# Optimization experiments

Measured on AMD Instinct MI355X. Metric: run time of the kernel, lower is better.

The kernel has to match this reference:

```python
import jax, jax.numpy as jnp
import numpy as np

B, S, D, H = 2, 2048, 1024, 16
HD = D // H  # head_dim = 64


def setup_inputs() -> dict:
    key = jax.random.key(0)
    ks = jax.random.split(key, 12)
    scale = 1.0 / np.sqrt(D)
    inp = {
        "query": jax.random.normal(ks[0], (B, S, D), jnp.float32),
        "key": jax.random.normal(ks[1], (B, S, D), jnp.float32),
        "value": jax.random.normal(ks[2], (B, S, D), jnp.float32),
        # causal mask, True = masked out; shape [B, q_len, k_len]
        "mask": jnp.broadcast_to(
            jnp.triu(jnp.ones((S, S), jnp.bool_), k=1), (B, S, S)
        ),
        "Wq": jax.random.normal(ks[3], (D, D), jnp.float32) * scale,
        "bq": jnp.zeros((D,), jnp.float32),
        "Wk": jax.random.normal(ks[4], (D, D), jnp.float32) * scale,
        "bk": jnp.zeros((D,), jnp.float32),
        "Wv": jax.random.normal(ks[5], (D, D), jnp.float32) * scale,
        "bv": jnp.zeros((D,), jnp.float32),
        "Wo": jax.random.normal(ks[6], (D, D), jnp.float32) * scale,
        "bo": jnp.zeros((D,), jnp.float32),
    }
    return inp


def _split_heads(x):
    b, s, _ = x.shape
    return x.reshape(b, s, H, HD).transpose(0, 2, 1, 3)  # [B,H,S,HD]


def reference(query, key, value, mask, Wq, bq, Wk, bk, Wv, bv, Wo, bo):
    # Linear layers use torch convention: y = x @ W.T + b, W is [out, in]
    q = _split_heads(query @ Wq.T + bq)
    k = _split_heads(key @ Wk.T + bk)
    v = _split_heads(value @ Wv.T + bv)
    scores = jnp.einsum("bhqd,bhkd->bhqk", q, k) / jnp.sqrt(jnp.float32(HD))
    # normalized mask [B,1,q,k]; True means masked
    scores = jnp.where(mask[:, None, :, :], jnp.finfo(scores.dtype).min, scores)
    attn = jax.nn.softmax(scores, axis=-1)  # dropout is identity in eval
    ctx = jnp.einsum("bhqk,bhkd->bhqd", attn, v)
    merged = ctx.transpose(0, 2, 1, 3).reshape(query.shape[0], -1, D)
    out = merged @ Wo.T + bo
    return out
```

## Files before the change

kernel.cpp:

```cpp
#include <hip/hip_runtime.h>

#define B_ 2
#define S_ 2048
#define D_ 1024
#define H_ 16
#define HD_ 64
#define M_ (B_ * S_)

typedef __bf16 bf16x8 __attribute__((ext_vector_type(8)));
typedef float f32x4 __attribute__((ext_vector_type(4)));

__device__ inline unsigned short f2bf(float f) {
    unsigned int u = __builtin_bit_cast(unsigned int, f);
    u += 0x7fffu + ((u >> 16) & 1u);
    return (unsigned short)(u >> 16);
}

__device__ inline unsigned int cvt_pk_bf16(float lo, float hi) {
    unsigned int r;
    asm("v_cvt_pk_bf16_f32 %0, %1, %2" : "=v"(r) : "v"(lo), "v"(hi));
    return r;
}

__device__ inline float fexp2(float x) { return __builtin_amdgcn_exp2f(x); }

__device__ inline void barrier_fence() {
    asm volatile("" ::: "memory");
    __builtin_amdgcn_s_barrier();
    asm volatile("" ::: "memory");
}

__device__ inline void async_ld16(const unsigned short* g, unsigned short* l) {
    __builtin_amdgcn_global_load_lds(
        (const __attribute__((address_space(1))) unsigned int*)g,
        (__attribute__((address_space(3))) unsigned int*)l, 16, 0, 0);
}

__global__ __launch_bounds__(256) void cvt_all(
    const float* __restrict__ i0, const float* __restrict__ i1, const float* __restrict__ i2,
    const float* __restrict__ i3, const float* __restrict__ i4, const float* __restrict__ i5,
    const float* __restrict__ i6,
    unsigned short* __restrict__ o0, unsigned short* __restrict__ o1, unsigned short* __restrict__ o2,
    unsigned short* __restrict__ o3, unsigned short* __restrict__ o4, unsigned short* __restrict__ o5,
    unsigned short* __restrict__ o6, int nbig, int nsmall) {
    int z = blockIdx.y;
    const float* in = (z == 0) ? i0 : (z == 1) ? i1 : (z == 2) ? i2 : (z == 3) ? i3
                     : (z == 4) ? i4 : (z == 5) ? i5 : i6;
    unsigned short* out = (z == 0) ? o0 : (z == 1) ? o1 : (z == 2) ? o2 : (z == 3) ? o3
                         : (z == 4) ? o4 : (z == 5) ? o5 : o6;
    int n = (z < 3) ? nbig : nsmall;
    int i = (blockIdx.x * 256 + threadIdx.x) * 4;
    if (i >= n) return;
    float4 v = *(const float4*)(in + i);
    ushort4 o;
    o.x = f2bf(v.x); o.y = f2bf(v.y); o.z = f2bf(v.z); o.w = f2bf(v.w);
    *(ushort4*)(out + i) = o;
}

__device__ inline void gemm_compute(const unsigned short* __restrict__ A,
                                    const unsigned short* __restrict__ W,
                                    int K, int m0, int n0,
                                    unsigned short* As0, unsigned short* As1,
                                    unsigned short* Bs0, unsigned short* Bs1,
                                    f32x4 acc[4][4]) {
    const int t = threadIdx.x;
    const int lane = t & 63, wave = t >> 6;
    const int ml = lane & 15, quad = lane >> 4;
    const int wr = (wave >> 1) * 64, wc = (wave & 1) * 64;
    const int srow = lane >> 2;
    const int schunk = (lane & 3) ^ ((lane >> 4) & 3);

    const f32x4 zero = {0.f, 0.f, 0.f, 0.f};
    for (int i = 0; i < 4; i++)
        for (int j = 0; j < 4; j++) acc[i][j] = zero;

    const int niter = K >> 5;

    auto issue = [&](int kt, unsigned short* As, unsigned short* Bs) {
        int k0 = kt << 5;
        for (int i = 0; i < 2; i++) {
            int r = wave * 32 + i * 16;
            async_ld16(A + (size_t)(m0 + r + srow) * K + k0 + schunk * 8, As + r * 32);
            async_ld16(W + (size_t)(n0 + r + srow) * K + k0 + schunk * 8, Bs + r * 32);
        }
    };

    issue(0, As0, Bs0);
    issue(1, As1, Bs1);
    asm volatile("s_waitcnt vmcnt(4)" ::: "memory");
    barrier_fence();

    for (int kt = 0; kt < niter; kt++) {
        unsigned short* As = (kt & 1) ? As1 : As0;
        unsigned short* Bs = (kt & 1) ? Bs1 : Bs0;

        bf16x8 af[4], bfr[4];
        for (int i = 0; i < 4; i++)
            af[i] = *(const bf16x8*)(As + (wr + i * 16 + ml) * 32 + ((quad ^ (ml >> 2)) << 3));
        for (int j = 0; j < 4; j++)
            bfr[j] = *(const bf16x8*)(Bs + (wc + j * 16 + ml) * 32 + ((quad ^ (ml >> 2)) << 3));
        for (int i = 0; i < 4; i++)
            for (int j = 0; j < 4; j++)
                acc[i][j] = __builtin_amdgcn_mfma_f32_16x16x32_bf16(af[i], bfr[j], acc[i][j], 0, 0, 0);

        barrier_fence();
        if (kt + 2 < niter) {
            issue(kt + 2, As, Bs);
            asm volatile("s_waitcnt vmcnt(4)" ::: "memory");
        } else {
            asm volatile("s_waitcnt vmcnt(0)" ::: "memory");
        }
        barrier_fence();
    }
}

__global__ __launch_bounds__(256) void gemm_qkv(
    const unsigned short* __restrict__ xq, const unsigned short* __restrict__ xk,
    const unsigned short* __restrict__ xv,
    const unsigned short* __restrict__ wq, const unsigned short* __restrict__ wk,
    const unsigned short* __restrict__ wv,
    const float* __restrict__ bq, const float* __restrict__ bk, const float* __restrict__ bv,
    unsigned short* __restrict__ oq, unsigned short* __restrict__ ok,
    unsigned short* __restrict__ ov) {
    extern __shared__ __align__(16) unsigned short smem[];
    unsigned short* As0 = smem;
    unsigned short* As1 = smem + 4096;
    unsigned short* Bs0 = smem + 8192;
    unsigned short* Bs1 = smem + 12288;

    int f = blockIdx.x + (blockIdx.y << 3) + (blockIdx.z << 8);
    int l = (f & 7) * 96 + (f >> 3);
    int bx = l & 7, by = (l >> 3) & 31, z = l >> 8;

    const unsigned short *A, *W;
    const float* bias;
    unsigned short* out;
    if (z == 0) { A = xq; W = wq; bias = bq; out = oq; }
    else if (z == 1) { A = xk; W = wk; bias = bk; out = ok; }
    else { A = xv; W = wv; bias = bv; out = ov; }

    int m0 = by * 128, n0 = bx * 128;
    f32x4 acc[4][4];
    gemm_compute(A, W, D_, m0, n0, As0, As1, Bs0, Bs1, acc);

    const int t = threadIdx.x, lane = t & 63, wave = t >> 6;
    const int ml = lane & 15, quad = lane >> 4;
    const int wr = (wave >> 1) * 64, wc = (wave & 1) * 64;

    unsigned short* Cs = smem;
    const float sc = (z == 0) ? 0.1803368801111204f : 1.0f;
    for (int i = 0; i < 4; i++)
        for (int j = 0; j < 4; j++) {
            int col = wc + j * 16 + ml;
            float bb = bias[n0 + col];
            for (int rg = 0; rg < 4; rg++) {
                int row = wr + i * 16 + quad * 4 + rg;
                unsigned short v = f2bf((acc[i][j][rg] + bb) * sc);
                if (z < 2) Cs[row * 136 + col] = v;
                else       Cs[col * 136 + row] = v;
            }
        }
    __syncthreads();

    const int r = t >> 1, hf = t & 1;
    if (z < 2) {
        unsigned short* dst = out + (size_t)(m0 + r) * D_ + n0 + hf * 64;
        const unsigned short* src = Cs + r * 136 + hf * 64;
        for (int i = 0; i < 8; i++)
            *(uint4*)(dst + i * 8) = *(const uint4*)(src + i * 8);
    } else {
        int n = n0 + r, h = n >> 6, d = n & 63;
        int b = m0 >> 11, s0 = m0 & 2047;
        unsigned short* dst = ov + ((size_t)((b * H_ + h) * 64 + d)) * S_ + s0 + hf * 64;
        const unsigned short* src = Cs + r * 136 + hf * 64;
        for (int i = 0; i < 8; i++)
            *(uint4*)(dst + i * 8) = *(const uint4*)(src + i * 8);
    }
}

__global__ __launch_bounds__(256) void gemm_out(const unsigned short* __restrict__ A,
                                                const unsigned short* __restrict__ W,
                                                const float* __restrict__ bias,
                                                float* __restrict__ out) {
    __shared__ unsigned short As0[128 * 32], As1[128 * 32], Bs0[128 * 32], Bs1[128 * 32];

    int f = blockIdx.x + (blockIdx.y << 3);
    int l = (f & 7) * 32 + (f >> 3);
    int bx = l & 7, by = l >> 3;

    int m0 = by * 128, n0 = bx * 128;
    f32x4 acc[4][4];
    gemm_compute(A, W, D_, m0, n0, As0, As1, Bs0, Bs1, acc);

    const int t = threadIdx.x, lane = t & 63, wave = t >> 6;
    const int ml = lane & 15, quad = lane >> 4;
    const int wr = (wave >> 1) * 64, wc = (wave & 1) * 64;
    for (int i = 0; i < 4; i++)
        for (int j = 0; j < 4; j++) {
            int n = n0 + wc + j * 16 + ml;
            float bb = bias[n];
            for (int rg = 0; rg < 4; rg++) {
                int m = m0 + wr + i * 16 + quad * 4 + rg;
                out[(size_t)m * D_ + n] = acc[i][j][rg] + bb;
            }
        }
}

__global__ __launch_bounds__(256, 2) void attn_kernel(const unsigned short* __restrict__ qm,
                                                      const unsigned short* __restrict__ km,
                                                      const unsigned short* __restrict__ vt,
                                                      unsigned short* __restrict__ ctx) {
    __shared__ unsigned short Ks[2][128 * 64];
    __shared__ unsigned short Vs[2][64 * 128];

    const int g = blockIdx.x >> 5;
    const int ip = (g < 8) ? (15 - g) : (g - 8);
    const int bh = blockIdx.x & 31;
    const int b = bh >> 4, h = bh & 15;
    const size_t vbase = (size_t)bh * S_ * 64;
    const int t = threadIdx.x, lane = t & 63, wave = t >> 6;
    const int ml = lane & 15, quad = lane >> 4;
    const int lrow = lane >> 3;
    const int gchunk = (lane & 7) ^ lrow;
    const int vrow = lane >> 4;
    const int q0 = ip * 128;
    const int nt = ip + 1;

    bf16x8 qfA[2], qfB[2];
    {
        int qrow = q0 + wave * 16 + ml;
        const unsigned short* qp = qm + (size_t)(b * S_ + qrow) * D_ + h * 64;
        qfA[0] = *(const bf16x8*)(qp + quad * 8);
        qfA[1] = *(const bf16x8*)(qp + 32 + quad * 8);
        const unsigned short* qp2 = qp + (size_t)64 * D_;
        qfB[0] = *(const bf16x8*)(qp2 + quad * 8);
        qfB[1] = *(const bf16x8*)(qp2 + 32 + quad * 8);
    }

    auto issue_K = [&](int kt, int bb) {
        for (int i = 0; i < 4; i++) {
            int r = wave * 32 + i * 8;
            async_ld16(km + (size_t)(b * S_ + kt * 128 + r + lrow) * D_ + h * 64 + gchunk * 8,
                       Ks[bb] + r * 64);
        }
    };
    auto issue_V = [&](int kt, int bb) {
        for (int i = 0; i < 4; i++) {
            int dd = wave * 16 + i * 4;
            int d = dd + vrow;
            async_ld16(vt + vbase + (size_t)d * S_ + kt * 128 + (((lane & 15) ^ (d & 15)) << 3),
                       Vs[bb] + dd * 128);
        }
    };

    const f32x4 zero = {0.f, 0.f, 0.f, 0.f};
    f32x4 accA[4], accB[4];
    for (int j = 0; j < 4; j++) { accA[j] = zero; accB[j] = zero; }
    float mA = -INFINITY, mB = -INFINITY, lpA = 0.f, lpB = 0.f;

    issue_K(0, 0);
    issue_V(0, 0);
    asm volatile("s_waitcnt vmcnt(0)" ::: "memory");
    barrier_fence();

    for (int kt = 0; kt < nt; kt++) {
        const int buf = kt & 1;
        if (kt + 1 < nt) { issue_K(kt + 1, buf ^ 1); issue_V(kt + 1, buf ^ 1); }

        f32x4 sA[8], sB[8];
        for (int n = 0; n < 8; n++) { sA[n] = zero; sB[n] = zero; }
        __builtin_amdgcn_s_setprio(1);
        for (int n = 0; n < 8; n++)
            for (int kk = 0; kk < 2; kk++) {
                bf16x8 kf = *(const bf16x8*)(Ks[buf] + (n * 16 + ml) * 64 +
                                             (((kk * 4 + quad) ^ (ml & 7)) << 3));
                sA[n] = __builtin_amdgcn_mfma_f32_16x16x32_bf16(kf, qfA[kk], sA[n], 0, 0, 0);
                sB[n] = __builtin_amdgcn_mfma_f32_16x16x32_bf16(kf, qfB[kk], sB[n], 0, 0, 0);
            }
        __builtin_amdgcn_s_setprio(0);

        const int qidxA = q0 + wave * 16 + ml;
        const int qidxB = qidxA + 64;
        if (kt == nt - 1) {
            for (int n = 0; n < 8; n++)
                for (int rg = 0; rg < 4; rg++) {
                    int kidx = kt * 128 + n * 16 + quad * 4 + rg;
                    if (kidx > qidxA) sA[n][rg] = -3.0e38f;
                    if (kidx > qidxB) sB[n][rg] = -3.0e38f;
                }
        }

        float a0 = fmaxf(fmaxf(sA[0][0], sA[0][1]), fmaxf(sA[0][2], sA[0][3]));
        float a1 = fmaxf(fmaxf(sA[1][0], sA[1][1]), fmaxf(sA[1][2], sA[1][3]));
        float a2 = fmaxf(fmaxf(sA[2][0], sA[2][1]), fmaxf(sA[2][2], sA[2][3]));
        float a3 = fmaxf(fmaxf(sA[3][0], sA[3][1]), fmaxf(sA[3][2], sA[3][3]));
        float a4 = fmaxf(fmaxf(sA[4][0], sA[4][1]), fmaxf(sA[4][2], sA[4][3]));
        float a5 = fmaxf(fmaxf(sA[5][0], sA[5][1]), fmaxf(sA[5][2], sA[5][3]));
        float a6 = fmaxf(fmaxf(sA[6][0], sA[6][1]), fmaxf(sA[6][2], sA[6][3]));
        float a7 = fmaxf(fmaxf(sA[7][0], sA[7][1]), fmaxf(sA[7][2], sA[7][3]));
        float mxA = fmaxf(fmaxf(fmaxf(a0, a1), fmaxf(a2, a3)),
                          fmaxf(fmaxf(a4, a5), fmaxf(a6, a7)));
        float b0 = fmaxf(fmaxf(sB[0][0], sB[0][1]), fmaxf(sB[0][2], sB[0][3]));
        float b1 = fmaxf(fmaxf(sB[1][0], sB[1][1]), fmaxf(sB[1][2], sB[1][3]));
        float b2 = fmaxf(fmaxf(sB[2][0], sB[2][1]), fmaxf(sB[2][2], sB[2][3]));
        float b3 = fmaxf(fmaxf(sB[3][0], sB[3][1]), fmaxf(sB[3][2], sB[3][3]));
        float b4 = fmaxf(fmaxf(sB[4][0], sB[4][1]), fmaxf(sB[4][2], sB[4][3]));
        float b5 = fmaxf(fmaxf(sB[5][0], sB[5][1]), fmaxf(sB[5][2], sB[5][3]));
        float b6 = fmaxf(fmaxf(sB[6][0], sB[6][1]), fmaxf(sB[6][2], sB[6][3]));
        float b7 = fmaxf(fmaxf(sB[7][0], sB[7][1]), fmaxf(sB[7][2], sB[7][3]));
        float mxB = fmaxf(fmaxf(fmaxf(b0, b1), fmaxf(b2, b3)),
                          fmaxf(fmaxf(b4, b5), fmaxf(b6, b7)));

        if (!__all((mxA <= mA + 4.0f) & (mxB <= mB + 4.0f))) {
            float mcA = fmaxf(mxA, __shfl_xor(mxA, 16));
            mcA = fmaxf(mcA, __shfl_xor(mcA, 32));
            mcA = fmaxf(mA, mcA);
            float alA = fexp2(mA - mcA);
            mA = mcA;
            float mcB = fmaxf(mxB, __shfl_xor(mxB, 16));
            mcB = fmaxf(mcB, __shfl_xor(mcB, 32));
            mcB = fmaxf(mB, mcB);
            float alB = fexp2(mB - mcB);
            mB = mcB;
            float aTA[4], aTB[4];
            for (int rg = 0; rg < 4; rg++) {
                aTA[rg] = __shfl(alA, quad * 4 + rg);
                aTB[rg] = __shfl(alB, quad * 4 + rg);
            }
            for (int j = 0; j < 4; j++)
                for (int rg = 0; rg < 4; rg++) {
                    accA[j][rg] *= aTA[rg];
                    accB[j][rg] *= aTB[rg];
                }
            lpA *= alA;
            lpB *= alB;
        }

        for (int n = 0; n < 8; n++)
            for (int rg = 0; rg < 4; rg++) {
                sA[n][rg] = fexp2(sA[n][rg] - mA);
                sB[n][rg] = fexp2(sB[n][rg] - mB);
            }
        {
            float r0 = 0.f, r1 = 0.f;
            for (int n = 0; n < 8; n++) {
                r0 += (sA[n][0] + sA[n][1]) + (sA[n][2] + sA[n][3]);
                r1 += (sB[n][0] + sB[n][1]) + (sB[n][2] + sB[n][3]);
            }
            lpA += r0;
            lpB += r1;
        }

        __builtin_amdgcn_s_setprio(1);
        for (int n2 = 0; n2 < 4; n2++) {
            union { bf16x8 v; unsigned int w[4]; } pkA, pkB;
            pkA.w[0] = cvt_pk_bf16(sA[2 * n2][0], sA[2 * n2][1]);
            pkA.w[1] = cvt_pk_bf16(sA[2 * n2][2], sA[2 * n2][3]);
            pkA.w[2] = cvt_pk_bf16(sA[2 * n2 + 1][0], sA[2 * n2 + 1][1]);
            pkA.w[3] = cvt_pk_bf16(sA[2 * n2 + 1][2], sA[2 * n2 + 1][3]);
            pkB.w[0] = cvt_pk_bf16(sB[2 * n2][0], sB[2 * n2][1]);
            pkB.w[1] = cvt_pk_bf16(sB[2 * n2][2], sB[2 * n2][3]);
            pkB.w[2] = cvt_pk_bf16(sB[2 * n2 + 1][0], sB[2 * n2 + 1][1]);
            pkB.w[3] = cvt_pk_bf16(sB[2 * n2 + 1][2], sB[2 * n2 + 1][3]);
            const int c0 = 4 * n2 + (quad >> 1);
            const int qo = (quad & 1) << 2;
            for (int j = 0; j < 4; j++) {
                int row = j * 16 + ml;
                union { bf16x8 v; uint2 d2[2]; } vv;
                vv.d2[0] = *(const uint2*)(Vs[buf] + row * 128 + (((c0 ^ (row & 15)) << 3) + qo));
                vv.d2[1] = *(const uint2*)(Vs[buf] + row * 128 + ((((c0 + 2) ^ (row & 15)) << 3) + qo));
                accA[j] = __builtin_amdgcn_mfma_f32_16x16x32_bf16(pkA.v, vv.v, accA[j], 0, 0, 0);
                accB[j] = __builtin_amdgcn_mfma_f32_16x16x32_bf16(pkB.v, vv.v, accB[j], 0, 0, 0);
            }
        }
        __builtin_amdgcn_s_setprio(0);

        asm volatile("s_waitcnt vmcnt(0)" ::: "memory");
        barrier_fence();
    }

    float lcA = lpA + __shfl_xor(lpA, 16);
    lcA += __shfl_xor(lcA, 32);
    float lcB = lpB + __shfl_xor(lpB, 16);
    lcB += __shfl_xor(lcB, 32);
    float invA[4], invB[4];
    for (int rg = 0; rg < 4; rg++) {
        invA[rg] = __builtin_amdgcn_rcpf(__shfl(lcA, quad * 4 + rg));
        invB[rg] = __builtin_amdgcn_rcpf(__shfl(lcB, quad * 4 + rg));
    }
    for (int j = 0; j < 4; j++) {
        int d = j * 16 + ml;
        for (int rg = 0; rg < 4; rg++) {
            int srow = q0 + wave * 16 + quad * 4 + rg;
            ctx[((size_t)(b * S_ + srow)) * D_ + h * 64 + d] = f2bf(accA[j][rg] * invA[rg]);
            ctx[((size_t)(b * S_ + srow + 64)) * D_ + h * 64 + d] = f2bf(accB[j][rg] * invB[rg]);
        }
    }
}

extern "C" void kernel_launch(void* const* d_in, const int* in_sizes, int n_in,
                              void* d_out, int out_size, void* d_ws, size_t ws_size,
                              hipStream_t stream) {
    const float* query = (const float*)d_in[0];
    const float* key_ = (const float*)d_in[1];
    const float* value = (const float*)d_in[2];
    const float* Wq = (const float*)d_in[4];
    const float* bq = (const float*)d_in[5];
    const float* Wk = (const float*)d_in[6];
    const float* bk = (const float*)d_in[7];
    const float* Wv = (const float*)d_in[8];
    const float* bv = (const float*)d_in[9];
    const float* Wo = (const float*)d_in[10];
    const float* bo = (const float*)d_in[11];
    float* out = (float*)d_out;

    const size_t XE = (size_t)M_ * D_;
    const size_t WE = (size_t)D_ * D_;
    char* ws = (char*)d_ws;
    unsigned short* xq = (unsigned short*)ws; ws += XE * 2;
    unsigned short* xk = (unsigned short*)ws; ws += XE * 2;
    unsigned short* xv = (unsigned short*)ws; ws += XE * 2;
    unsigned short* wqb = (unsigned short*)ws; ws += WE * 2;
    unsigned short* wkb = (unsigned short*)ws; ws += WE * 2;
    unsigned short* wvb = (unsigned short*)ws; ws += WE * 2;
    unsigned short* wob = (unsigned short*)ws; ws += WE * 2;
    unsigned short* qmb = (unsigned short*)ws; ws += XE * 2;
    unsigned short* kmb = (unsigned short*)ws; ws += XE * 2;
    unsigned short* vt = (unsigned short*)ws; ws += XE * 2;
    unsigned short* ctx = (unsigned short*)ws; ws += XE * 2;

    cvt_all<<<dim3(XE / 1024, 7), 256, 0, stream>>>(
        query, key_, value, Wq, Wk, Wv, Wo,
        xq, xk, xv, wqb, wkb, wvb, wob, (int)XE, (int)WE);

    gemm_qkv<<<dim3(D_ / 128, M_ / 128, 3), 256, 34816, stream>>>(
        xq, xk, xv, wqb, wkb, wvb, bq, bk, bv, qmb, kmb, vt);

    attn_kernel<<<dim3(512), 256, 0, stream>>>(qmb, kmb, vt, ctx);

    gemm_out<<<dim3(D_ / 128, M_ / 128), 256, 0, stream>>>(ctx, wob, bo, out);
}
```

Baseline: 245.6 us.

## Fuse fp32-to-bf16 conversion into GEMM loads, dropping the separate cvt kernel

Removes the standalone conversion kernel that wrote bf16 copies of the inputs and weights. The QKV and output GEMMs now load fp32 directly into registers, pack to bf16 with v_cvt_pk_bf16, and write to LDS through a register-staged double buffer. The output GEMM keeps async global-to-LDS loads for the bf16 context. This saves a kernel launch and a write-then-reread round trip, but the GEMMs now read twice as many bytes and give up direct-to-LDS async loads, so latency hiding inside the main loop may get worse.

```diff
diff --git a/kernel.cpp b/kernel.cpp
--- a/kernel.cpp
+++ b/kernel.cpp
@@ -30,39 +30,38 @@
     asm volatile("" ::: "memory");
 }
 
+__device__ inline void order_fence() {
+    asm volatile("" ::: "memory");
+}
+
 __device__ inline void async_ld16(const unsigned short* g, unsigned short* l) {
     __builtin_amdgcn_global_load_lds(
         (const __attribute__((address_space(1))) unsigned int*)g,
         (__attribute__((address_space(3))) unsigned int*)l, 16, 0, 0);
 }
 
-__global__ __launch_bounds__(256) void cvt_all(
-    const float* __restrict__ i0, const float* __restrict__ i1, const float* __restrict__ i2,
-    const float* __restrict__ i3, const float* __restrict__ i4, const float* __restrict__ i5,
-    const float* __restrict__ i6,
-    unsigned short* __restrict__ o0, unsigned short* __restrict__ o1, unsigned short* __restrict__ o2,
-    unsigned short* __restrict__ o3, unsigned short* __restrict__ o4, unsigned short* __restrict__ o5,
-    unsigned short* __restrict__ o6, int nbig, int nsmall) {
-    int z = blockIdx.y;
-    const float* in = (z == 0) ? i0 : (z == 1) ? i1 : (z == 2) ? i2 : (z == 3) ? i3
-                     : (z == 4) ? i4 : (z == 5) ? i5 : i6;
-    unsigned short* out = (z == 0) ? o0 : (z == 1) ? o1 : (z == 2) ? o2 : (z == 3) ? o3
-                         : (z == 4) ? o4 : (z == 5) ? o5 : o6;
-    int n = (z < 3) ? nbig : nsmall;
-    int i = (blockIdx.x * 256 + threadIdx.x) * 4;
-    if (i >= n) return;
-    float4 v = *(const float4*)(in + i);
-    ushort4 o;
-    o.x = f2bf(v.x); o.y = f2bf(v.y); o.z = f2bf(v.z); o.w = f2bf(v.w);
-    *(ushort4*)(out + i) = o;
-}
-
-__device__ inline void gemm_compute(const unsigned short* __restrict__ A,
-                                    const unsigned short* __restrict__ W,
-                                    int K, int m0, int n0,
-                                    unsigned short* As0, unsigned short* As1,
-                                    unsigned short* Bs0, unsigned short* Bs1,
-                                    f32x4 acc[4][4]) {
+struct f32x8r { float4 lo, hi; };
+__device__ inline f32x8r ldg8(const float* p) {
+    f32x8r r;
+    r.lo = *(const float4*)p;
+    r.hi = *(const float4*)(p + 4);
+    return r;
+}
+__device__ inline uint4 pk8(const f32x8r& v) {
+    uint4 o;
+    o.x = cvt_pk_bf16(v.lo.x, v.lo.y);
+    o.y = cvt_pk_bf16(v.lo.z, v.lo.w);
+    o.z = cvt_pk_bf16(v.hi.x, v.hi.y);
+    o.w = cvt_pk_bf16(v.hi.z, v.hi.w);
+    return o;
+}
+
+__device__ inline void gemm_compute_f32(const float* __restrict__ A,
+                                        const float* __restrict__ W,
+                                        int K, int m0, int n0,
+                                        unsigned short* As0, unsigned short* As1,
+                                        unsigned short* Bs0, unsigned short* Bs1,
+                                        f32x4 acc[4][4]) {
     const int t = threadIdx.x;
     const int lane = t & 63, wave = t >> 6;
     const int ml = lane & 15, quad = lane >> 4;
@@ -76,23 +75,43 @@
 
     const int niter = K >> 5;
 
-    auto issue = [&](int kt, unsigned short* As, unsigned short* Bs) {
+    const float* pA0 = A + (size_t)(m0 + wave * 32 + srow) * K + schunk * 8;
+    const float* pA1 = pA0 + (size_t)16 * K;
+    const float* pW0 = W + (size_t)(n0 + wave * 32 + srow) * K + schunk * 8;
+    const float* pW1 = pW0 + (size_t)16 * K;
+    const int woff = wave * 32 * 32 + lane * 8;
+
+    f32x8r rA0, rA1, rW0, rW1;
+    auto LOAD = [&](int kt) {
         int k0 = kt << 5;
-        for (int i = 0; i < 2; i++) {
-            int r = wave * 32 + i * 16;
-            async_ld16(A + (size_t)(m0 + r + srow) * K + k0 + schunk * 8, As + r * 32);
-            async_ld16(W + (size_t)(n0 + r + srow) * K + k0 + schunk * 8, Bs + r * 32);
-        }
-    };
-
-    issue(0, As0, Bs0);
-    issue(1, As1, Bs1);
-    asm volatile("s_waitcnt vmcnt(4)" ::: "memory");
+        rA0 = ldg8(pA0 + k0);
+        rA1 = ldg8(pA1 + k0);
+        rW0 = ldg8(pW0 + k0);
+        rW1 = ldg8(pW1 + k0);
+    };
+    auto WRITE = [&](unsigned short* As, unsigned short* Bs) {
+        *(uint4*)(As + woff) = pk8(rA0);
+        *(uint4*)(As + woff + 512) = pk8(rA1);
+        *(uint4*)(Bs + woff) = pk8(rW0);
+        *(uint4*)(Bs + woff + 512) = pk8(rW1);
+    };
+
+    LOAD(0);
+    asm volatile("s_waitcnt vmcnt(0)" ::: "memory");
+    WRITE(As0, Bs0);
+    LOAD(1);
+    asm volatile("s_waitcnt lgkmcnt(0)" ::: "memory");
     barrier_fence();
 
     for (int kt = 0; kt < niter; kt++) {
         unsigned short* As = (kt & 1) ? As1 : As0;
         unsigned short* Bs = (kt & 1) ? Bs1 : Bs0;
+
+        if (kt + 1 < niter) {
+            asm volatile("s_waitcnt vmcnt(0)" ::: "memory");
+            WRITE((kt & 1) ? As0 : As1, (kt & 1) ? Bs0 : Bs1);
+            if (kt + 2 < niter) LOAD(kt + 2);
+        }
 
         bf16x8 af[4], bfr[4];
         for (int i = 0; i < 4; i++)
@@ -103,22 +122,96 @@
             for (int j = 0; j < 4; j++)
                 acc[i][j] = __builtin_amdgcn_mfma_f32_16x16x32_bf16(af[i], bfr[j], acc[i][j], 0, 0, 0);
 
+        asm volatile("s_waitcnt lgkmcnt(0)" ::: "memory");
         barrier_fence();
-        if (kt + 2 < niter) {
-            issue(kt + 2, As, Bs);
-            asm volatile("s_waitcnt vmcnt(4)" ::: "memory");
-        } else {
+    }
+}
+
+__device__ inline void gemm_compute_mix(const unsigned short* __restrict__ A,
+                                        const float* __restrict__ W,
+                                        int K, int m0, int n0,
+                                        unsigned short* As0, unsigned short* As1,
+                                        unsigned short* Bs0, unsigned short* Bs1,
+                                        f32x4 acc[4][4]) {
+    const int t = threadIdx.x;
+    const int lane = t & 63, wave = t >> 6;
+    const int ml = lane & 15, quad = lane >> 4;
+    const int wr = (wave >> 1) * 64, wc = (wave & 1) * 64;
+    const int srow = lane >> 2;
+    const int schunk = (lane & 3) ^ ((lane >> 4) & 3);
+
+    const f32x4 zero = {0.f, 0.f, 0.f, 0.f};
+    for (int i = 0; i < 4; i++)
+        for (int j = 0; j < 4; j++) acc[i][j] = zero;
+
+    const int niter = K >> 5;
+
+    const float* pW0 = W + (size_t)(n0 + wave * 32 + srow) * K + schunk * 8;
+    const float* pW1 = pW0 + (size_t)16 * K;
+    const int woff = wave * 32 * 32 + lane * 8;
+
+    f32x8r rW0, rW1;
+    auto LOADW = [&](int kt) {
+        int k0 = kt << 5;
+        rW0 = ldg8(pW0 + k0);
+        rW1 = ldg8(pW1 + k0);
+    };
+    auto WRITEW = [&](unsigned short* Bs) {
+        *(uint4*)(Bs + woff) = pk8(rW0);
+        *(uint4*)(Bs + woff + 512) = pk8(rW1);
+    };
+    auto issueA = [&](int kt, unsigned short* As) {
+        int k0 = kt << 5;
+        for (int i = 0; i < 2; i++) {
+            int r = wave * 32 + i * 16;
+            async_ld16(A + (size_t)(m0 + r + srow) * K + k0 + schunk * 8, As + r * 32);
+        }
+    };
+
+    LOADW(0);
+    asm volatile("s_waitcnt vmcnt(0)" ::: "memory");
+    WRITEW(Bs0);
+    issueA(0, As0);
+    order_fence();
+    LOADW(1);
+    asm volatile("s_waitcnt vmcnt(4)" ::: "memory");
+    asm volatile("s_waitcnt lgkmcnt(0)" ::: "memory");
+    barrier_fence();
+
+    for (int kt = 0; kt < niter; kt++) {
+        unsigned short* As = (kt & 1) ? As1 : As0;
+        unsigned short* Bs = (kt & 1) ? Bs1 : Bs0;
+
+        const bool more = (kt + 1 < niter);
+        if (more) {
             asm volatile("s_waitcnt vmcnt(0)" ::: "memory");
-        }
+            WRITEW((kt & 1) ? Bs0 : Bs1);
+            issueA(kt + 1, (kt & 1) ? As0 : As1);
+            order_fence();
+            if (kt + 2 < niter) LOADW(kt + 2);
+        }
+
+        bf16x8 af[4], bfr[4];
+        for (int i = 0; i < 4; i++)
+            af[i] = *(const bf16x8*)(As + (wr + i * 16 + ml) * 32 + ((quad ^ (ml >> 2)) << 3));
+        for (int j = 0; j < 4; j++)
+            bfr[j] = *(const bf16x8*)(Bs + (wc + j * 16 + ml) * 32 + ((quad ^ (ml >> 2)) << 3));
+        for (int i = 0; i < 4; i++)
+            for (int j = 0; j < 4; j++)
+                acc[i][j] = __builtin_amdgcn_mfma_f32_16x16x32_bf16(af[i], bfr[j], acc[i][j], 0, 0, 0);
+
+        if (more && kt + 2 < niter) asm volatile("s_waitcnt vmcnt(4)" ::: "memory");
+        else                        asm volatile("s_waitcnt vmcnt(0)" ::: "memory");
+        asm volatile("s_waitcnt lgkmcnt(0)" ::: "memory");
         barrier_fence();
     }
 }
 
 __global__ __launch_bounds__(256) void gemm_qkv(
-    const unsigned short* __restrict__ xq, const unsigned short* __restrict__ xk,
-    const unsigned short* __restrict__ xv,
-    const unsigned short* __restrict__ wq, const unsigned short* __restrict__ wk,
-    const unsigned short* __restrict__ wv,
+    const float* __restrict__ xq, const float* __restrict__ xk,
+    const float* __restrict__ xv,
+    const float* __restrict__ wq, const float* __restrict__ wk,
+    const float* __restrict__ wv,
     const float* __restrict__ bq, const float* __restrict__ bk, const float* __restrict__ bv,
     unsigned short* __restrict__ oq, unsigned short* __restrict__ ok,
     unsigned short* __restrict__ ov) {
@@ -132,7 +225,7 @@
     int l = (f & 7) * 96 + (f >> 3);
     int bx = l & 7, by = (l >> 3) & 31, z = l >> 8;
 
-    const unsigned short *A, *W;
+    const float *A, *W;
     const float* bias;
     unsigned short* out;
     if (z == 0) { A = xq; W = wq; bias = bq; out = oq; }
@@ -141,7 +234,7 @@
 
     int m0 = by * 128, n0 = bx * 128;
     f32x4 acc[4][4];
-    gemm_compute(A, W, D_, m0, n0, As0, As1, Bs0, Bs1, acc);
+    gemm_compute_f32(A, W, D_, m0, n0, As0, As1, Bs0, Bs1, acc);
 
     const int t = threadIdx.x, lane = t & 63, wave = t >> 6;
     const int ml = lane & 15, quad = lane >> 4;
@@ -179,7 +272,7 @@
 }
 
 __global__ __launch_bounds__(256) void gemm_out(const unsigned short* __restrict__ A,
-                                                const unsigned short* __restrict__ W,
+                                                const float* __restrict__ W,
                                                 const float* __restrict__ bias,
                                                 float* __restrict__ out) {
     __shared__ unsigned short As0[128 * 32], As1[128 * 32], Bs0[128 * 32], Bs1[128 * 32];
@@ -190,7 +283,7 @@
 
     int m0 = by * 128, n0 = bx * 128;
     f32x4 acc[4][4];
-    gemm_compute(A, W, D_, m0, n0, As0, As1, Bs0, Bs1, acc);
+    gemm_compute_mix(A, W, D_, m0, n0, As0, As1, Bs0, Bs1, acc);
 
     const int t = threadIdx.x, lane = t & 63, wave = t >> 6;
     const int ml = lane & 15, quad = lane >> 4;
@@ -415,28 +508,16 @@
     float* out = (float*)d_out;
 
     const size_t XE = (size_t)M_ * D_;
-    const size_t WE = (size_t)D_ * D_;
     char* ws = (char*)d_ws;
-    unsigned short* xq = (unsigned short*)ws; ws += XE * 2;
-    unsigned short* xk = (unsigned short*)ws; ws += XE * 2;
-    unsigned short* xv = (unsigned short*)ws; ws += XE * 2;
-    unsigned short* wqb = (unsigned short*)ws; ws += WE * 2;
-    unsigned short* wkb = (unsigned short*)ws; ws += WE * 2;
-    unsigned short* wvb = (unsigned short*)ws; ws += WE * 2;
-    unsigned short* wob = (unsigned short*)ws; ws += WE * 2;
     unsigned short* qmb = (unsigned short*)ws; ws += XE * 2;
     unsigned short* kmb = (unsigned short*)ws; ws += XE * 2;
     unsigned short* vt = (unsigned short*)ws; ws += XE * 2;
     unsigned short* ctx = (unsigned short*)ws; ws += XE * 2;
 
-    cvt_all<<<dim3(XE / 1024, 7), 256, 0, stream>>>(
-        query, key_, value, Wq, Wk, Wv, Wo,
-        xq, xk, xv, wqb, wkb, wvb, wob, (int)XE, (int)WE);
-
     gemm_qkv<<<dim3(D_ / 128, M_ / 128, 3), 256, 34816, stream>>>(
-        xq, xk, xv, wqb, wkb, wvb, bq, bk, bv, qmb, kmb, vt);
+        query, key_, value, Wq, Wk, Wv, bq, bk, bv, qmb, kmb, vt);
 
     attn_kernel<<<dim3(512), 256, 0, stream>>>(qmb, kmb, vt, ctx);
 
-    gemm_out<<<dim3(D_ / 128, M_ / 128), 256, 0, stream>>>(ctx, wob, bo, out);
-}
+    gemm_out<<<dim3(D_ / 128, M_ / 128), 256, 0, stream>>>(ctx, Wo, bo, out);
+}
```

Measured after the change: 264.4 us. +7.7%, slower.

## Enlarge QKV projection GEMM tile to 256x128 with two-pass epilogue

Applied to the files above, without the earlier changes.

The QKV projection GEMM moves from 128x128 to 256x128 tiles, with each wave computing a 128x64 sub-tile. This raises arithmetic intensity and reuse of the B operand. The epilogue writes results through shared memory in two halves so the existing staging buffer size still fits. The cost is fewer blocks (384 instead of 768), more accumulator registers per wave, and a larger LDS footprint, which may reduce occupancy and worsen wave-quantization tail effects.

```diff
diff --git a/kernel.cpp b/kernel.cpp
--- a/kernel.cpp
+++ b/kernel.cpp
@@ -114,7 +114,67 @@
     }
 }
 
-__global__ __launch_bounds__(256) void gemm_qkv(
+__device__ inline void gemm_compute256(const unsigned short* __restrict__ A,
+                                       const unsigned short* __restrict__ W,
+                                       int K, int m0, int n0,
+                                       unsigned short* As0, unsigned short* As1,
+                                       unsigned short* Bs0, unsigned short* Bs1,
+                                       f32x4 acc[8][4]) {
+    const int t = threadIdx.x;
+    const int lane = t & 63, wave = t >> 6;
+    const int ml = lane & 15, quad = lane >> 4;
+    const int wr = (wave >> 1) * 128, wc = (wave & 1) * 64;
+    const int srow = lane >> 2;
+    const int schunk = (lane & 3) ^ ((lane >> 4) & 3);
+
+    const f32x4 zero = {0.f, 0.f, 0.f, 0.f};
+    for (int i = 0; i < 8; i++)
+        for (int j = 0; j < 4; j++) acc[i][j] = zero;
+
+    const int niter = K >> 5;
+
+    auto issue = [&](int kt, unsigned short* As, unsigned short* Bs) {
+        int k0 = kt << 5;
+        for (int i = 0; i < 4; i++) {
+            int r = wave * 64 + i * 16;
+            async_ld16(A + (size_t)(m0 + r + srow) * K + k0 + schunk * 8, As + r * 32);
+        }
+        for (int i = 0; i < 2; i++) {
+            int r = wave * 32 + i * 16;
+            async_ld16(W + (size_t)(n0 + r + srow) * K + k0 + schunk * 8, Bs + r * 32);
+        }
+    };
+
+    issue(0, As0, Bs0);
+    issue(1, As1, Bs1);
+    asm volatile("s_waitcnt vmcnt(6)" ::: "memory");
+    barrier_fence();
+
+    for (int kt = 0; kt < niter; kt++) {
+        unsigned short* As = (kt & 1) ? As1 : As0;
+        unsigned short* Bs = (kt & 1) ? Bs1 : Bs0;
+
+        bf16x8 bfr[4];
+        for (int j = 0; j < 4; j++)
+            bfr[j] = *(const bf16x8*)(Bs + (wc + j * 16 + ml) * 32 + ((quad ^ (ml >> 2)) << 3));
+        for (int i = 0; i < 8; i++) {
+            bf16x8 af = *(const bf16x8*)(As + (wr + i * 16 + ml) * 32 + ((quad ^ (ml >> 2)) << 3));
+            for (int j = 0; j < 4; j++)
+                acc[i][j] = __builtin_amdgcn_mfma_f32_16x16x32_bf16(af, bfr[j], acc[i][j], 0, 0, 0);
+        }
+
+        barrier_fence();
+        if (kt + 2 < niter) {
+            issue(kt + 2, As, Bs);
+            asm volatile("s_waitcnt vmcnt(6)" ::: "memory");
+        } else {
+            asm volatile("s_waitcnt vmcnt(0)" ::: "memory");
+        }
+        barrier_fence();
+    }
+}
+
+__global__ __launch_bounds__(256, 2) void gemm_qkv(
     const unsigned short* __restrict__ xq, const unsigned short* __restrict__ xk,
     const unsigned short* __restrict__ xv,
     const unsigned short* __restrict__ wq, const unsigned short* __restrict__ wk,
@@ -124,13 +184,13 @@
     unsigned short* __restrict__ ov) {
     extern __shared__ __align__(16) unsigned short smem[];
     unsigned short* As0 = smem;
-    unsigned short* As1 = smem + 4096;
-    unsigned short* Bs0 = smem + 8192;
-    unsigned short* Bs1 = smem + 12288;
-
-    int f = blockIdx.x + (blockIdx.y << 3) + (blockIdx.z << 8);
-    int l = (f & 7) * 96 + (f >> 3);
-    int bx = l & 7, by = (l >> 3) & 31, z = l >> 8;
+    unsigned short* As1 = smem + 8192;
+    unsigned short* Bs0 = smem + 16384;
+    unsigned short* Bs1 = smem + 20480;
+
+    int f = blockIdx.x + (blockIdx.y << 3) + (blockIdx.z << 7);
+    int l = (f & 7) * 48 + (f >> 3);
+    int bx = l & 7, by = (l >> 3) & 15, z = l >> 7;
 
     const unsigned short *A, *W;
     const float* bias;
@@ -139,42 +199,49 @@
     else if (z == 1) { A = xk; W = wk; bias = bk; out = ok; }
     else { A = xv; W = wv; bias = bv; out = ov; }
 
-    int m0 = by * 128, n0 = bx * 128;
-    f32x4 acc[4][4];
-    gemm_compute(A, W, D_, m0, n0, As0, As1, Bs0, Bs1, acc);
+    int m0 = by * 256, n0 = bx * 128;
+    f32x4 acc[8][4];
+    gemm_compute256(A, W, D_, m0, n0, As0, As1, Bs0, Bs1, acc);
 
     const int t = threadIdx.x, lane = t & 63, wave = t >> 6;
     const int ml = lane & 15, quad = lane >> 4;
-    const int wr = (wave >> 1) * 64, wc = (wave & 1) * 64;
+    const int wc = (wave & 1) * 64;
+    const int whalf = wave >> 1;
 
     unsigned short* Cs = smem;
     const float sc = (z == 0) ? 0.1803368801111204f : 1.0f;
-    for (int i = 0; i < 4; i++)
-        for (int j = 0; j < 4; j++) {
-            int col = wc + j * 16 + ml;
-            float bb = bias[n0 + col];
-            for (int rg = 0; rg < 4; rg++) {
-                int row = wr + i * 16 + quad * 4 + rg;
-                unsigned short v = f2bf((acc[i][j][rg] + bb) * sc);
-                if (z < 2) Cs[row * 136 + col] = v;
-                else       Cs[col * 136 + row] = v;
-            }
-        }
-    __syncthreads();
-
     const int r = t >> 1, hf = t & 1;
-    if (z < 2) {
-        unsigned short* dst = out + (size_t)(m0 + r) * D_ + n0 + hf * 64;
-        const unsigned short* src = Cs + r * 136 + hf * 64;
-        for (int i = 0; i < 8; i++)
-            *(uint4*)(dst + i * 8) = *(const uint4*)(src + i * 8);
-    } else {
-        int n = n0 + r, h = n >> 6, d = n & 63;
-        int b = m0 >> 11, s0 = m0 & 2047;
-        unsigned short* dst = ov + ((size_t)((b * H_ + h) * 64 + d)) * S_ + s0 + hf * 64;
-        const unsigned short* src = Cs + r * 136 + hf * 64;
-        for (int i = 0; i < 8; i++)
-            *(uint4*)(dst + i * 8) = *(const uint4*)(src + i * 8);
+
+    for (int p = 0; p < 2; p++) {
+        if (whalf == p) {
+            for (int i = 0; i < 8; i++)
+                for (int j = 0; j < 4; j++) {
+                    int col = wc + j * 16 + ml;
+                    float bb = bias[n0 + col];
+                    for (int rg = 0; rg < 4; rg++) {
+                        int lrow = i * 16 + quad * 4 + rg;
+                        unsigned short v = f2bf((acc[i][j][rg] + bb) * sc);
+                        if (z < 2) Cs[lrow * 136 + col] = v;
+                        else       Cs[col * 136 + lrow] = v;
+                    }
+                }
+        }
+        __syncthreads();
+
+        if (z < 2) {
+            unsigned short* dst = out + (size_t)(m0 + p * 128 + r) * D_ + n0 + hf * 64;
+            const unsigned short* src = Cs + r * 136 + hf * 64;
+            for (int i = 0; i < 8; i++)
+                *(uint4*)(dst + i * 8) = *(const uint4*)(src + i * 8);
+        } else {
+            int n = n0 + r, h = n >> 6, d = n & 63;
+            int b = m0 >> 11, s0 = (m0 & 2047) + p * 128;
+            unsigned short* dst = ov + ((size_t)((b * H_ + h) * 64 + d)) * S_ + s0 + hf * 64;
+            const unsigned short* src = Cs + r * 136 + hf * 64;
+            for (int i = 0; i < 8; i++)
+                *(uint4*)(dst + i * 8) = *(const uint4*)(src + i * 8);
+        }
+        __syncthreads();
     }
 }
 
@@ -433,7 +500,7 @@
         query, key_, value, Wq, Wk, Wv, Wo,
         xq, xk, xv, wqb, wkb, wvb, wob, (int)XE, (int)WE);
 
-    gemm_qkv<<<dim3(D_ / 128, M_ / 128, 3), 256, 34816, stream>>>(
+    gemm_qkv<<<dim3(8, 16, 3), 256, 49152, stream>>>(
         xq, xk, xv, wqb, wkb, wvb, bq, bk, bv, qmb, kmb, vt);
 
     attn_kernel<<<dim3(512), 256, 0, stream>>>(qmb, kmb, vt, ctx);
```

After: 275.0 us. 12.0% more time.
